# Kernel tuning notes

Measured on AMD Instinct MI355X. Metric: run time of the kernel, lower is better.

The kernel has to match this reference:

```python
import jax, jax.numpy as jnp
import numpy as np

E, D, H = 8, 1024, 4096  # num_experts, backbone hidden, moe hidden
B, S = 4, 4096
TEMPERATURE = 1.0


def setup_inputs() -> dict:
    key = jax.random.key(0)
    ks = jax.random.split(key, 7)
    sc = 0.02
    return {
        "x": jax.random.normal(ks[0], (B, S, D), dtype=jnp.float32),
        "W1": jax.random.normal(ks[1], (E, D, H), dtype=jnp.float32) * sc,
        "b1": jax.random.normal(ks[2], (E, H), dtype=jnp.float32) * sc,
        "W2": jax.random.normal(ks[3], (E, H, D), dtype=jnp.float32) * sc,
        "b2": jax.random.normal(ks[4], (E, D), dtype=jnp.float32) * sc,
        "Wr": jax.random.normal(ks[5], (D, E), dtype=jnp.float32) * sc,
        "br": jax.random.normal(ks[6], (E,), dtype=jnp.float32) * sc,
    }


def reference(x, W1, b1, W2, b2, Wr, br):
    # Router: logits -> temperature -> softmax -> top-1 expert index per token
    routing_logits = (x @ Wr + br) / TEMPERATURE          # [B,S,E]
    routing_probs = jax.nn.softmax(routing_logits, axis=-1)
    indices = jnp.argmax(routing_probs, axis=-1)          # [B,S] (top-1)

    # Faithful to source: every expert runs on the masked (zeroed) inputs,
    # so each expert's bias path expert_i(0) is added for every token.
    out = jnp.zeros_like(x)
    num_experts = W1.shape[0]
    for i in range(num_experts):  # fixed small loop over experts
        mask = (indices == i).astype(x.dtype)[..., None]  # [B,S,1]
        xi = x * mask                                     # [B,S,D]
        h = jax.nn.relu(xi @ W1[i] + b1[i])               # [B,S,H]
        out = out + (h @ W2[i] + b2[i])                   # [B,S,D]
    return out
```

## Files before the change

### kernel.cpp

```cpp
#include <hip/hip_runtime.h>
#include <cstdint>

#define E_ 8
#define D_ 1024
#define H_ 4096
#define NTOK 16384

typedef unsigned short ushort_t;
typedef __attribute__((ext_vector_type(8))) short short8;
typedef __attribute__((ext_vector_type(4))) float f32x4;

__device__ __forceinline__ ushort_t f2bf(float f) {
  uint32_t u = __builtin_bit_cast(uint32_t, f);
  uint32_t r = (u + 0x7fffu + ((u >> 16) & 1u)) >> 16;
  return (ushort_t)r;
}

__device__ __forceinline__ void gload_lds16(const void* g, void* l) {
  __builtin_amdgcn_global_load_lds(
      (const __attribute__((address_space(1))) uint32_t*)g,
      (__attribute__((address_space(3))) uint32_t*)l, 16, 0, 0);
}

__global__ void init_kernel(int* cursor, float* rawbase) {
  int tid = threadIdx.x + blockIdx.x * 256;
  if (tid < 8) cursor[tid] = 0;
  if (tid < E_ * D_) rawbase[tid] = 0.f;
}

template <int FUSE>
__global__ void transpose_bf16(const float* __restrict__ in, ushort_t* __restrict__ out,
                               int R, int C, const float* __restrict__ b1,
                               float* __restrict__ rawbase) {
  __shared__ ushort_t t[64][70];
  __shared__ float scs[16][64];
  __shared__ float relu_b1[64];
  const int e = blockIdx.z;
  const float* ip = in + (size_t)e * R * C;
  ushort_t* op = out + (size_t)e * R * C;
  const int c0 = blockIdx.x * 64, r0 = blockIdx.y * 64;
  const int tid = threadIdx.x;
  if (FUSE) {
    if (tid < 64) relu_b1[tid] = fmaxf(b1[e * R + r0 + tid], 0.f);
    __syncthreads();
  }
  const int rsub = tid >> 4;
  const int c4 = (tid & 15) * 4;
  float s0 = 0.f, s1 = 0.f, s2 = 0.f, s3 = 0.f;
#pragma unroll
  for (int q = 0; q < 4; ++q) {
    int r = q * 16 + rsub;
    float4 v = *(const float4*)&ip[(size_t)(r0 + r) * C + c0 + c4];
    t[c4 + 0][r] = f2bf(v.x);
    t[c4 + 1][r] = f2bf(v.y);
    t[c4 + 2][r] = f2bf(v.z);
    t[c4 + 3][r] = f2bf(v.w);
    if (FUSE) {
      float rb = relu_b1[r];
      s0 += rb * v.x; s1 += rb * v.y; s2 += rb * v.z; s3 += rb * v.w;
    }
  }
  if (FUSE) {
    scs[rsub][c4 + 0] = s0; scs[rsub][c4 + 1] = s1;
    scs[rsub][c4 + 2] = s2; scs[rsub][c4 + 3] = s3;
  }
  __syncthreads();
  if (FUSE && tid < 64) {
    float tot = 0.f;
#pragma unroll
    for (int g = 0; g < 16; ++g) tot += scs[g][tid];
    atomicAdd(&rawbase[e * D_ + c0 + tid], tot);
  }
#pragma unroll
  for (int it = 0; it < 2; ++it) {
    int idx = it * 256 + tid;
    int c = idx >> 3, g = idx & 7;
    short8 v;
#pragma unroll
    for (int k = 0; k < 8; ++k) v[k] = (short)t[c][g * 8 + k];
    *(short8*)&op[(size_t)(c0 + c) * R + r0 + g * 8] = v;
  }
}

__global__ void adj_kernel(const float* __restrict__ rawbase, const float* __restrict__ b2,
                           float* __restrict__ adj) {
  int i = blockIdx.x * 256 + threadIdx.x;
  int d = i & (D_ - 1);
  int e = i >> 10;
  float tot = 0.f;
#pragma unroll
  for (int ii = 0; ii < E_; ++ii) tot += rawbase[ii * D_ + d] + b2[ii * D_ + d];
  adj[i] = tot - rawbase[e * D_ + d];
}

__global__ void router_kernel(const float* __restrict__ x, const float* __restrict__ Wr,
                              const float* __restrict__ br, int* __restrict__ idx) {
  __shared__ float wr_s[E_][D_];
  const int tid = threadIdx.x;
  for (int j = tid; j < E_ * D_; j += 256) {
    int e = j & 7, d = j >> 3;
    wr_s[e][d] = Wr[j];
  }
  __syncthreads();
  const int wid = tid >> 6, l = tid & 63;
  const int t0 = blockIdx.x * 32 + wid * 8;
  for (int tt = 0; tt < 8; ++tt) {
    int t = t0 + tt;
    const float4* xr4 = (const float4*)(x + (size_t)t * D_);
    float s[E_];
#pragma unroll
    for (int e = 0; e < E_; ++e) s[e] = 0.f;
#pragma unroll
    for (int q = 0; q < 4; ++q) {
      float4 xv = xr4[q * 64 + l];
#pragma unroll
      for (int e = 0; e < E_; ++e) {
        const float4 wv = *(const float4*)&wr_s[e][(q * 64 + l) * 4];
        s[e] += xv.x * wv.x + xv.y * wv.y + xv.z * wv.z + xv.w * wv.w;
      }
    }
#pragma unroll
    for (int e = 0; e < E_; ++e) {
#pragma unroll
      for (int off = 32; off > 0; off >>= 1) s[e] += __shfl_xor(s[e], off, 64);
    }
    if (l == 0) {
      float best = s[0] + br[0];
      int bi = 0;
#pragma unroll
      for (int e = 1; e < E_; ++e) {
        float v = s[e] + br[e];
        if (v > best) { best = v; bi = e; }
      }
      idx[t] = bi;
    }
  }
}

__global__ void count_scan_build(const int* __restrict__ idx, int* __restrict__ offsets,
                                 int* __restrict__ work1, int* __restrict__ work2,
                                 int* __restrict__ meta) {
  __shared__ int hist[256][E_];
  __shared__ int nt[E_], b1s[E_], b2s[E_];
  const int tid = threadIdx.x;
  int c[E_];
#pragma unroll
  for (int e = 0; e < E_; ++e) c[e] = 0;
  for (int t = tid; t < NTOK; t += 256) ++c[idx[t]];
#pragma unroll
  for (int e = 0; e < E_; ++e) hist[tid][e] = c[e];
  __syncthreads();
  if (tid == 0) {
    int acc = 0, w1 = 0, w2 = 0;
    for (int e = 0; e < E_; ++e) {
      int s = 0;
      for (int i = 0; i < 256; ++i) s += hist[i][e];
      offsets[e] = acc;
      acc += s;
      int n = (s + 255) >> 8;
      nt[e] = n;
      b1s[e] = w1; w1 += n * (H_ / 256);
      b2s[e] = w2; w2 += n * (D_ / 256);
    }
    offsets[E_] = acc;
    meta[0] = w1;
    meta[1] = w2;
  }
  __syncthreads();
  if (tid < E_) {
    const int e = tid, n = nt[e];
    int p = b1s[e];
    for (int tn = 0; tn < H_ / 256; ++tn)
      for (int tm = 0; tm < n; ++tm)
        work1[p++] = (e << 16) | (tm << 8) | tn;
  } else if (tid < 2 * E_) {
    const int e = tid - E_, n = nt[e];
    int p = b2s[e];
    for (int tn = 0; tn < D_ / 256; ++tn)
      for (int tm = 0; tm < n; ++tm)
        work2[p++] = (e << 16) | (tm << 8) | tn;
  }
}

__global__ void scatter_kernel(const float* __restrict__ x, const int* __restrict__ idx,
                               const int* __restrict__ offsets, int* __restrict__ cursor,
                               int* __restrict__ perm, ushort_t* __restrict__ xg) {
  __shared__ int slots[64];
  const int tid = threadIdx.x;
  const int t0 = blockIdx.x * 64;
  if (tid < 64) {
    const int t = t0 + tid;
    const int e = idx[t];
    const unsigned long long lanebit = 1ull << tid;
    int slot = 0;
#pragma unroll
    for (int ee = 0; ee < E_; ++ee) {
      unsigned long long m = __ballot(e == ee);
      if (e == ee) {
        int lead = __ffsll((long long)m) - 1;
        int base = 0;
        if (tid == lead) base = atomicAdd(&cursor[ee], __popcll(m));
        base = __shfl(base, lead, 64);
        slot = offsets[ee] + base + __popcll(m & (lanebit - 1));
      }
    }
    slots[tid] = slot;
    perm[slot] = t;
  }
  __syncthreads();
  for (int r = 0; r < 64; ++r) {
    const int t = t0 + r;
    const int slot = slots[r];
    float4 v = *(const float4*)(x + (size_t)t * D_ + tid * 4);
    ushort4 o;
    o.x = f2bf(v.x); o.y = f2bf(v.y); o.z = f2bf(v.z); o.w = f2bf(v.w);
    *(ushort4*)(xg + (size_t)slot * D_ + tid * 4) = o;
  }
}


template <int MODE>
__global__ __launch_bounds__(512, 2) void ffn_gemm(
    const ushort_t* __restrict__ A_all, const ushort_t* __restrict__ Bw,
    const float* __restrict__ bias, const int* __restrict__ offs,
    const int* __restrict__ perm, float* __restrict__ out, ushort_t* __restrict__ hbo,
    const int* __restrict__ work, const int* __restrict__ nw_p) {
  constexpr int KdF = (MODE == 1) ? D_ : H_;
  constexpr int Nd = (MODE == 1) ? H_ : D_;
  constexpr int NKT = KdF / 32;

  const int n1 = *nw_p;
  int bid = blockIdx.x;
  if (bid >= n1) return;
  {
    int q = n1 >> 3, r = n1 & 7;
    int xcd = bid & 7, pos = bid >> 3;
    bid = (xcd < r ? xcd * (q + 1) : r * (q + 1) + (xcd - r) * q) + pos;
  }
  const int item = work[bid];
  const int e = (item >> 16) & 255, tm = (item >> 8) & 255, tn = item & 255;
  const int ms = offs[e];
  const int M = offs[e + 1] - ms;

  __shared__ __align__(16) ushort_t lds[4][2][8192];

  const int tid = threadIdx.x;
  const int wid = tid >> 6, l = tid & 63;
  const int wm = wid >> 2, wn = wid & 3;
  const int lr = l & 15, lh = l >> 4;

  const ushort_t* Ab = A_all + (size_t)ms * KdF;
  const ushort_t* Bb = Bw + (size_t)e * ((size_t)Nd * KdF);
  const int arow0 = tm * 256;
  const int brow0 = tn * 256;
  const int rowmaxA = M - 1;

  int a_src[2], b_src[2];
#pragma unroll
  for (int c = 0; c < 2; ++c) {
    int s = c * 512 + tid;
    int P = s >> 3, U = s & 7;
    int Ur = U ^ (P & 7);
    int r = 2 * P + (Ur >> 2);
    int u = Ur & 3;
    int ga = arow0 + r;
    if (ga > rowmaxA) ga = rowmaxA;
    a_src[c] = ga * KdF + u * 8;
    b_src[c] = (brow0 + r) * KdF + u * 8;
  }

#define STAGE(buf, kt)                                                                   \
  _Pragma("unroll") for (int c_ = 0; c_ < 2; ++c_) {                                     \
    gload_lds16(Ab + a_src[c_] + (kt) * 32, &lds[buf][0][(c_ * 512 + wid * 64) * 8]);    \
    gload_lds16(Bb + b_src[c_] + (kt) * 32, &lds[buf][1][(c_ * 512 + wid * 64) * 8]);    \
  }

#define AOFF(r) (((((r) >> 1)) << 6) + ((((lh) + (((r) & 1) << 2)) ^ (((r) >> 1) & 7)) << 3))

  f32x4 acc[8][4];
#pragma unroll
  for (int i = 0; i < 8; ++i)
#pragma unroll
    for (int j = 0; j < 4; ++j) acc[i][j] = (f32x4){0.f, 0.f, 0.f, 0.f};

  STAGE(0, 0)
  STAGE(1, 1)
  STAGE(2, 2)
  asm volatile("s_waitcnt vmcnt(8)" ::: "memory");
  __builtin_amdgcn_s_barrier();

#pragma unroll 4
  for (int kt = 0; kt < NKT; ++kt) {
    int pf = kt + 3;
    if (pf > NKT - 1) pf = NKT - 1;
    STAGE((kt + 3) & 3, pf)
    const ushort_t* la = &lds[kt & 3][0][0];
    const ushort_t* lb = &lds[kt & 3][1][0];
    short8 af[8], bq[4];
#pragma unroll
    for (int i = 0; i < 8; ++i)
      af[i] = *(const short8*)&la[AOFF(wm * 128 + i * 16 + lr)];
#pragma unroll
    for (int j = 0; j < 4; ++j)
      bq[j] = *(const short8*)&lb[AOFF(wn * 64 + j * 16 + lr)];
#pragma unroll
    for (int i = 0; i < 8; ++i)
#pragma unroll
      for (int j = 0; j < 4; ++j)
        acc[i][j] = __builtin_amdgcn_mfma_f32_16x16x32_bf16(af[i], bq[j], acc[i][j], 0, 0, 0);
    asm volatile("s_waitcnt vmcnt(8)" ::: "memory");
    __builtin_amdgcn_s_barrier();
  }

  const int gcolbase = tn * 256 + wn * 64 + lr;
  float bv[4];
#pragma unroll
  for (int j = 0; j < 4; ++j) bv[j] = bias[e * Nd + gcolbase + j * 16];
#pragma unroll
  for (int i = 0; i < 8; ++i) {
#pragma unroll
    for (int rr = 0; rr < 4; ++rr) {
      int grow = tm * 256 + wm * 128 + i * 16 + lh * 4 + rr;
      if (grow < M) {
        if (MODE == 1) {
          size_t rowoff = (size_t)(ms + grow) * H_;
#pragma unroll
          for (int j = 0; j < 4; ++j) {
            float v = acc[i][j][rr] + bv[j];
            v = fmaxf(v, 0.f);
            hbo[rowoff + gcolbase + j * 16] = f2bf(v);
          }
        } else {
          int tok = perm[ms + grow];
          size_t rowoff = (size_t)tok * D_;
#pragma unroll
          for (int j = 0; j < 4; ++j)
            out[rowoff + gcolbase + j * 16] = acc[i][j][rr] + bv[j];
        }
      }
    }
  }
#undef STAGE
#undef AOFF
}

extern "C" void kernel_launch(void* const* d_in, const int* in_sizes, int n_in,
                              void* d_out, int out_size, void* d_ws, size_t ws_size,
                              hipStream_t stream) {
  const float* x  = (const float*)d_in[0];
  const float* W1 = (const float*)d_in[1];
  const float* b1 = (const float*)d_in[2];
  const float* W2 = (const float*)d_in[3];
  const float* b2 = (const float*)d_in[4];
  const float* Wr = (const float*)d_in[5];
  const float* br = (const float*)d_in[6];
  float* out = (float*)d_out;

  char* ws = (char*)d_ws;
  ushort_t* W1t   = (ushort_t*)(ws);
  ushort_t* W2t   = (ushort_t*)(ws + 67108864);
  ushort_t* xg    = (ushort_t*)(ws + 134217728);
  ushort_t* hb    = (ushort_t*)(ws + 167772160);
  float*    rawbase = (float*)(ws + 301989888);
  float*    adj   = (float*)(ws + 302022656);
  int*      idx   = (int*)(ws + 302055424);
  int*      perm  = (int*)(ws + 302120960);
  int*      cursor = (int*)(ws + 302186496);
  int*      offsets = (int*)(ws + 302186624);
  int*      meta   = (int*)(ws + 302186752);
  int*      work1  = (int*)(ws + 302186880);
  int*      work2  = (int*)(ws + 302195072);

  init_kernel<<<32, 256, 0, stream>>>(cursor, rawbase);
  transpose_bf16<0><<<dim3(H_ / 64, D_ / 64, E_), 256, 0, stream>>>(W1, W1t, D_, H_,
                                                                    nullptr, nullptr);
  transpose_bf16<1><<<dim3(D_ / 64, H_ / 64, E_), 256, 0, stream>>>(W2, W2t, H_, D_,
                                                                    b1, rawbase);
  adj_kernel<<<32, 256, 0, stream>>>(rawbase, b2, adj);
  router_kernel<<<512, 256, 0, stream>>>(x, Wr, br, idx);
  count_scan_build<<<1, 256, 0, stream>>>(idx, offsets, work1, work2, meta);
  scatter_kernel<<<NTOK / 64, 256, 0, stream>>>(x, idx, offsets, cursor, perm, xg);
  ffn_gemm<1><<<1136, 512, 0, stream>>>(xg, W1t, b1, offsets, nullptr, nullptr, hb,
                                        work1, meta + 0);
  ffn_gemm<2><<<284, 512, 0, stream>>>(hb, W2t, adj, offsets, perm, out, nullptr,
                                       work2, meta + 1);
}
```

Measured before the change: 605.3 us.

## Replace atomic scatter with in-scan permutation and gather rows inside first GEMM

Builds the token permutation deterministically inside the single-block count/scan kernel using per-thread prefix offsets, which removes the cursor atomics. The scatter kernel is replaced by a plain contiguous fp32-to-bf16 conversion of x. The first FFN GEMM now loads A rows indirectly through perm, so a separate gathered copy of x is no longer written. The single-block kernel now does more serial work for the permutation, and the GEMM A loads become gathered rows rather than contiguous ones.

```diff
diff --git a/kernel.cpp b/kernel.cpp
--- a/kernel.cpp
+++ b/kernel.cpp
@@ -22,9 +22,8 @@
       (__attribute__((address_space(3))) uint32_t*)l, 16, 0, 0);
 }
 
-__global__ void init_kernel(int* cursor, float* rawbase) {
+__global__ void init_kernel(float* rawbase) {
   int tid = threadIdx.x + blockIdx.x * 256;
-  if (tid < 8) cursor[tid] = 0;
   if (tid < E_ * D_) rawbase[tid] = 0.f;
 }
 
@@ -139,9 +138,12 @@
 
 __global__ void count_scan_build(const int* __restrict__ idx, int* __restrict__ offsets,
                                  int* __restrict__ work1, int* __restrict__ work2,
-                                 int* __restrict__ meta) {
+                                 int* __restrict__ meta, int* __restrict__ perm) {
   __shared__ int hist[256][E_];
+  __shared__ int pb[256][E_];
+  __shared__ int esum[E_];
   __shared__ int nt[E_], b1s[E_], b2s[E_];
+  __shared__ int offs_s[E_];
   const int tid = threadIdx.x;
   int c[E_];
 #pragma unroll
@@ -149,13 +151,31 @@
   for (int t = tid; t < NTOK; t += 256) ++c[idx[t]];
 #pragma unroll
   for (int e = 0; e < E_; ++e) hist[tid][e] = c[e];
+  __syncthreads();
+  {
+    const int hw = tid >> 5, l32 = tid & 31;
+    int carry = 0;
+#pragma unroll
+    for (int ch = 0; ch < 8; ++ch) {
+      int v = hist[ch * 32 + l32][hw];
+      int s = v;
+#pragma unroll
+      for (int off = 1; off < 32; off <<= 1) {
+        int t = __shfl_up(s, off, 32);
+        if (l32 >= off) s += t;
+      }
+      pb[ch * 32 + l32][hw] = carry + s - v;
+      carry += __shfl(s, 31, 32);
+    }
+    if (l32 == 0) esum[hw] = carry;
+  }
   __syncthreads();
   if (tid == 0) {
     int acc = 0, w1 = 0, w2 = 0;
     for (int e = 0; e < E_; ++e) {
-      int s = 0;
-      for (int i = 0; i < 256; ++i) s += hist[i][e];
+      int s = esum[e];
       offsets[e] = acc;
+      offs_s[e] = acc;
       acc += s;
       int n = (s + 255) >> 8;
       nt[e] = n;
@@ -167,6 +187,11 @@
     meta[1] = w2;
   }
   __syncthreads();
+  for (int t = tid; t < NTOK; t += 256) {
+    int e = idx[t];
+    int p = pb[tid][e]++;
+    perm[offs_s[e] + p] = t;
+  }
   if (tid < E_) {
     const int e = tid, n = nt[e];
     int p = b1s[e];
@@ -182,40 +207,15 @@
   }
 }
 
-__global__ void scatter_kernel(const float* __restrict__ x, const int* __restrict__ idx,
-                               const int* __restrict__ offsets, int* __restrict__ cursor,
-                               int* __restrict__ perm, ushort_t* __restrict__ xg) {
-  __shared__ int slots[64];
-  const int tid = threadIdx.x;
-  const int t0 = blockIdx.x * 64;
-  if (tid < 64) {
-    const int t = t0 + tid;
-    const int e = idx[t];
-    const unsigned long long lanebit = 1ull << tid;
-    int slot = 0;
-#pragma unroll
-    for (int ee = 0; ee < E_; ++ee) {
-      unsigned long long m = __ballot(e == ee);
-      if (e == ee) {
-        int lead = __ffsll((long long)m) - 1;
-        int base = 0;
-        if (tid == lead) base = atomicAdd(&cursor[ee], __popcll(m));
-        base = __shfl(base, lead, 64);
-        slot = offsets[ee] + base + __popcll(m & (lanebit - 1));
-      }
-    }
-    slots[tid] = slot;
-    perm[slot] = t;
-  }
-  __syncthreads();
-  for (int r = 0; r < 64; ++r) {
-    const int t = t0 + r;
-    const int slot = slots[r];
-    float4 v = *(const float4*)(x + (size_t)t * D_ + tid * 4);
-    ushort4 o;
-    o.x = f2bf(v.x); o.y = f2bf(v.y); o.z = f2bf(v.z); o.w = f2bf(v.w);
-    *(ushort4*)(xg + (size_t)slot * D_ + tid * 4) = o;
-  }
+__global__ void convert_kernel(const float* __restrict__ x, ushort_t* __restrict__ xb) {
+  const size_t i = ((size_t)blockIdx.x * 256 + threadIdx.x) * 8;
+  float4 v0 = *(const float4*)(x + i);
+  float4 v1 = *(const float4*)(x + i + 4);
+  ushort4 o0, o1;
+  o0.x = f2bf(v0.x); o0.y = f2bf(v0.y); o0.z = f2bf(v0.z); o0.w = f2bf(v0.w);
+  o1.x = f2bf(v1.x); o1.y = f2bf(v1.y); o1.z = f2bf(v1.z); o1.w = f2bf(v1.w);
+  *(ushort4*)(xb + i) = o0;
+  *(ushort4*)(xb + i + 4) = o1;
 }
 
 
@@ -249,13 +249,13 @@
   const int wm = wid >> 2, wn = wid & 3;
   const int lr = l & 15, lh = l >> 4;
 
-  const ushort_t* Ab = A_all + (size_t)ms * KdF;
   const ushort_t* Bb = Bw + (size_t)e * ((size_t)Nd * KdF);
   const int arow0 = tm * 256;
   const int brow0 = tn * 256;
   const int rowmaxA = M - 1;
 
-  int a_src[2], b_src[2];
+  size_t a_src[2];
+  int b_src[2];
 #pragma unroll
   for (int c = 0; c < 2; ++c) {
     int s = c * 512 + tid;
@@ -265,13 +265,14 @@
     int u = Ur & 3;
     int ga = arow0 + r;
     if (ga > rowmaxA) ga = rowmaxA;
-    a_src[c] = ga * KdF + u * 8;
+    int arow = (MODE == 1) ? perm[ms + ga] : (ms + ga);
+    a_src[c] = (size_t)arow * KdF + u * 8;
     b_src[c] = (brow0 + r) * KdF + u * 8;
   }
 
 #define STAGE(buf, kt)                                                                   \
   _Pragma("unroll") for (int c_ = 0; c_ < 2; ++c_) {                                     \
-    gload_lds16(Ab + a_src[c_] + (kt) * 32, &lds[buf][0][(c_ * 512 + wid * 64) * 8]);    \
+    gload_lds16(A_all + a_src[c_] + (kt) * 32, &lds[buf][0][(c_ * 512 + wid * 64) * 8]); \
     gload_lds16(Bb + b_src[c_] + (kt) * 32, &lds[buf][1][(c_ * 512 + wid * 64) * 8]);    \
   }
 
@@ -359,28 +360,27 @@
   char* ws = (char*)d_ws;
   ushort_t* W1t   = (ushort_t*)(ws);
   ushort_t* W2t   = (ushort_t*)(ws + 67108864);
-  ushort_t* xg    = (ushort_t*)(ws + 134217728);
+  ushort_t* xb    = (ushort_t*)(ws + 134217728);
   ushort_t* hb    = (ushort_t*)(ws + 167772160);
   float*    rawbase = (float*)(ws + 301989888);
   float*    adj   = (float*)(ws + 302022656);
   int*      idx   = (int*)(ws + 302055424);
   int*      perm  = (int*)(ws + 302120960);
-  int*      cursor = (int*)(ws + 302186496);
   int*      offsets = (int*)(ws + 302186624);
   int*      meta   = (int*)(ws + 302186752);
   int*      work1  = (int*)(ws + 302186880);
   int*      work2  = (int*)(ws + 302195072);
 
-  init_kernel<<<32, 256, 0, stream>>>(cursor, rawbase);
+  init_kernel<<<32, 256, 0, stream>>>(rawbase);
   transpose_bf16<0><<<dim3(H_ / 64, D_ / 64, E_), 256, 0, stream>>>(W1, W1t, D_, H_,
                                                                     nullptr, nullptr);
   transpose_bf16<1><<<dim3(D_ / 64, H_ / 64, E_), 256, 0, stream>>>(W2, W2t, H_, D_,
                                                                     b1, rawbase);
   adj_kernel<<<32, 256, 0, stream>>>(rawbase, b2, adj);
   router_kernel<<<512, 256, 0, stream>>>(x, Wr, br, idx);
-  count_scan_build<<<1, 256, 0, stream>>>(idx, offsets, work1, work2, meta);
-  scatter_kernel<<<NTOK / 64, 256, 0, stream>>>(x, idx, offsets, cursor, perm, xg);
-  ffn_gemm<1><<<1136, 512, 0, stream>>>(xg, W1t, b1, offsets, nullptr, nullptr, hb,
+  count_scan_build<<<1, 256, 0, stream>>>(idx, offsets, work1, work2, meta, perm);
+  convert_kernel<<<NTOK * D_ / (256 * 8), 256, 0, stream>>>(x, xb);
+  ffn_gemm<1><<<1136, 512, 0, stream>>>(xb, W1t, b1, offsets, perm, nullptr, hb,
                                         work1, meta + 0);
   ffn_gemm<2><<<284, 512, 0, stream>>>(hb, W2t, adj, offsets, perm, out, nullptr,
                                        work2, meta + 1);
```

Result: no change. 600.5 us (-0.8%).
